# Performance work log

Measured on AMD Instinct MI355X. Metric: run time of the kernel, lower is better.

Reference implementation:

```python
import jax, jax.numpy as jnp
import numpy as np

B, S, D = 1, 2048, 3072
H, DH = 24, 128
ENC, NIP = 512, 64
COND = (512 // 8) * (512 // 8) * 16 // 64  # 1024 cond tokens per lora
RANK, ALPHA, LW, IP_SCALE = 16, 16.0, 1.0, 1.0
EPS = 1e-5


def _rms(x):
    return x * jax.lax.rsqrt(jnp.mean(x * x, axis=-1, keepdims=True) + EPS)


def _to_heads(x):
    b, s, _ = x.shape
    return x.reshape(b, s, H, DH).transpose(0, 2, 1, 3)  # [B,H,S,DH]


def _from_heads(x):
    b, h, s, d = x.shape
    return x.transpose(0, 2, 1, 3).reshape(b, s, h * d)


def _lora(x, dn, up):
    # token mask keeps only the cond block (number=0, n_loras=1 -> last COND tokens)
    y = ((x[:, -COND:, :] @ dn) @ up) * (ALPHA / RANK)
    z = jnp.zeros((x.shape[0], x.shape[1] - COND, up.shape[1]), x.dtype)
    return jnp.concatenate([z, y], axis=1)


def _sdpa(q, k, v, mask=None):
    s = jnp.einsum('bhqd,bhkd->bhqk', q, k) * (1.0 / np.sqrt(DH))
    if mask is not None:
        s = s + mask
    return jnp.einsum('bhqk,bhkd->bhqd', jax.nn.softmax(s, axis=-1), v)


def _forward(hidden_states, encoder_hidden_states, image_emb,
             Wq, bq, Wk, bk, Wv, bv, Waq, baq, Wak, bak, Wav, bav,
             Wo, bo, Wao, bao, Wkip, Wvip,
             lq_dn, lq_up, lk_dn, lk_up, lv_dn, lv_up, lp_dn, lp_up):
    hs, ehs, img = hidden_states, encoder_hidden_states, image_emb
    # context (encoder) projections + RMSNorm on q/k
    eq = _rms(_to_heads(ehs @ Waq + baq))
    ek = _rms(_to_heads(ehs @ Wak + bak))
    ev = _to_heads(ehs @ Wav + bav)
    # main-stream q/k/v with masked LoRA branches
    q = hs @ Wq + bq + LW * _lora(hs, lq_dn, lq_up)
    k = hs @ Wk + bk + LW * _lora(hs, lk_dn, lk_up)
    v = hs @ Wv + bv + LW * _lora(hs, lv_dn, lv_up)
    q = _rms(_to_heads(q))
    k = _rms(_to_heads(k))
    v = _to_heads(v)
    # IP-adapter branch: extra K/V from image_emb, norm_added_k is RMSNorm(128)
    kip = _rms(_to_heads(img @ Wkip))
    vip = _to_heads(img @ Wvip)
    ip_out = _from_heads(_sdpa(q, kip, vip))  # [B,S,D]
    # concat encoder stream ahead of main stream
    q = jnp.concatenate([eq, q], axis=2)
    k = jnp.concatenate([ek, k], axis=2)
    v = jnp.concatenate([ev, v], axis=2)
    SL = ENC + S
    SB = SL - COND  # scaled_block_size
    m = jnp.ones((SL, SL), jnp.float32)
    m = m.at[:SB, :].set(0.0)        # non-cond rows attend everywhere
    m = m.at[SB:, SB:].set(0.0)      # single cond block attends to itself (n_loras=1)
    mask = m * (-1e20)
    out = _from_heads(_sdpa(q, k, v, mask))  # [B,SL,D]
    enc_out = out[:, :ENC, :]
    main = out[:, ENC:, :] + IP_SCALE * ip_out
    main = main @ Wo + bo
    main = main + LW * _lora(main, lp_dn, lp_up)  # proj LoRA (to_out dropout=identity)
    enc_out = enc_out @ Wao + bao
    return jnp.concatenate([enc_out, main], axis=1)  # [B, ENC+S, D]


def setup_inputs():
    key = jax.random.key(0)
    ks = iter(jax.random.split(key, 40))
    w = lambda *sh: jax.random.normal(next(ks), sh, jnp.float32) * 0.02
    return dict(
        hidden_states=jax.random.normal(next(ks), (B, S, D), jnp.float32),
        encoder_hidden_states=jax.random.normal(next(ks), (B, ENC, D), jnp.float32),
        image_emb=jax.random.normal(next(ks), (B, NIP, D), jnp.float32),
        Wq=w(D, D), bq=w(D), Wk=w(D, D), bk=w(D), Wv=w(D, D), bv=w(D),
        Waq=w(D, D), baq=w(D), Wak=w(D, D), bak=w(D), Wav=w(D, D), bav=w(D),
        Wo=w(D, D), bo=w(D), Wao=w(D, D), bao=w(D),
        Wkip=w(D, D), Wvip=w(D, D),
        lq_dn=w(D, RANK), lq_up=w(RANK, D), lk_dn=w(D, RANK), lk_up=w(RANK, D),
        lv_dn=w(D, RANK), lv_up=w(RANK, D), lp_dn=w(D, RANK), lp_up=w(RANK, D),
    )


def reference(hidden_states, encoder_hidden_states, image_emb,
              Wq, bq, Wk, bk, Wv, bv, Waq, baq, Wak, bak, Wav, bav,
              Wo, bo, Wao, bao, Wkip, Wvip,
              lq_dn, lq_up, lk_dn, lk_up, lv_dn, lv_up, lp_dn, lp_up):
    return _forward(hidden_states, encoder_hidden_states, image_emb,
                    Wq, bq, Wk, bk, Wv, bv, Waq, baq, Wak, bak, Wav, bav,
                    Wo, bo, Wao, bao, Wkip, Wvip,
                    lq_dn, lq_up, lk_dn, lk_up, lv_dn, lv_up, lp_dn, lp_up)
```

## Files before the change

### kernel.cpp

```cpp
#include <hip/hip_runtime.h>

typedef unsigned short u16;
typedef short s16x8 __attribute__((ext_vector_type(8)));
typedef float f32x4 __attribute__((ext_vector_type(4)));
typedef const __attribute__((address_space(1))) unsigned int* as1_u32p;
typedef __attribute__((address_space(3))) unsigned int* as3_u32p;

static_assert(sizeof(s16x8) == 16, "");

struct alignas(8) U16x4 { u16 x, y, z, w; };

__device__ __forceinline__ u16 f2bf(float f) {
  union { float f; unsigned u; } c; c.f = f;
  return (u16)((c.u + 0x7fffu + ((c.u >> 16) & 1u)) >> 16);
}
__device__ __forceinline__ float bf2f(u16 h) {
  union { unsigned u; float f; } c; c.u = ((unsigned)h) << 16;
  return c.f;
}
__device__ __forceinline__ void async16(const void* g, void* l) {
  __builtin_amdgcn_global_load_lds((as1_u32p)g, (as3_u32p)l, 16, 0, 0);
}

__launch_bounds__(256)
__global__ void mega_prep(const float* __restrict__ Waq, const float* __restrict__ Wak,
                          const float* __restrict__ Wav, const float* __restrict__ Wq,
                          const float* __restrict__ Wk, const float* __restrict__ Wv,
                          u16* __restrict__ WTbE, u16* __restrict__ WTbM,
                          const float* __restrict__ Wo, const float* __restrict__ bo,
                          const float* __restrict__ lp_dn, float* __restrict__ Wod,
                          const float* __restrict__ d0, const float* __restrict__ d1,
                          const float* __restrict__ d2, float* __restrict__ tl,
                          const float* __restrict__ hs, u16* __restrict__ hsb,
                          const float* __restrict__ ehs, u16* __restrict__ ehsb,
                          const float* __restrict__ img, u16* __restrict__ imgb,
                          const float* __restrict__ baq, const float* __restrict__ bak,
                          const float* __restrict__ bav, const float* __restrict__ bq,
                          const float* __restrict__ bk, const float* __restrict__ bv,
                          float* __restrict__ bpk,
                          const float* __restrict__ u0, const float* __restrict__ u1,
                          const float* __restrict__ u2) {
  __shared__ char lmem[16896];
  const int b = blockIdx.x;
  const int tid = threadIdx.x;
  if (b < 13824) {
    int mat = b / 2304, tile = b % 2304;
    const float* src = (mat == 0) ? Waq : (mat == 1) ? Wak : (mat == 2) ? Wav
                       : (mat == 3) ? Wq : (mat == 4) ? Wk : Wv;
    u16* dst = (mat < 3) ? WTbE + (long)mat * 3072 * 3072
                         : WTbM + (long)(mat - 3) * 3072 * 3136;
    const int ldd = (mat < 3) ? 3072 : 3136;
    float (*tile2)[32][33] = (float(*)[32][33])lmem;
    int k0 = (tile / 96) * 128, n0 = (tile % 96) * 32;
    int r = tid >> 3, c4 = (tid & 7) * 4;
    float4 v[4];
#pragma unroll
    for (int t = 0; t < 4; ++t)
      v[t] = *(const float4*)(src + (long)(k0 + 32 * t + r) * 3072 + n0 + c4);
#pragma unroll
    for (int t = 0; t < 4; ++t) {
      tile2[t][r][c4 + 0] = v[t].x; tile2[t][r][c4 + 1] = v[t].y;
      tile2[t][r][c4 + 2] = v[t].z; tile2[t][r][c4 + 3] = v[t].w;
    }
    __syncthreads();
#pragma unroll
    for (int t = 0; t < 4; ++t) {
      U16x4 o{f2bf(tile2[t][c4 + 0][r]), f2bf(tile2[t][c4 + 1][r]),
              f2bf(tile2[t][c4 + 2][r]), f2bf(tile2[t][c4 + 3][r])};
      *(U16x4*)(dst + (long)(n0 + r) * ldd + k0 + 32 * t + c4) = o;
    }
  } else if (b < 14848) {
    const int m = b - 13824;
    float (*red)[48] = (float(*)[48])lmem;
    const float* xr = hs + (long)(1024 + m) * 3072;
    float p[48];
#pragma unroll
    for (int r = 0; r < 48; ++r) p[r] = 0.f;
    for (int k = tid; k < 3072; k += 256) {
      float a = xr[k];
      const float* e0 = d0 + (long)k * 16;
      const float* e1 = d1 + (long)k * 16;
      const float* e2 = d2 + (long)k * 16;
#pragma unroll
      for (int r = 0; r < 16; ++r) {
        p[r]      += a * e0[r];
        p[16 + r] += a * e1[r];
        p[32 + r] += a * e2[r];
      }
    }
#pragma unroll
    for (int r = 0; r < 48; ++r)
#pragma unroll
      for (int st = 1; st < 64; st <<= 1) p[r] += __shfl_xor(p[r], st, 64);
    int lane = tid & 63, w = tid >> 6;
    if (lane == 0) {
#pragma unroll
      for (int r = 0; r < 48; ++r) red[w][r] = p[r];
    }
    __syncthreads();
    if (tid < 48) {
      int r = tid;
      tl[(long)m * 48 + r] = red[0][r] + red[1][r] + red[2][r] + red[3][r];
    }
  } else if (b < 17921) {
    const int m = b - 14848;
    float (*red)[16] = (float(*)[16])lmem;
    const float* xr = (m < 3072) ? Wo + (long)m * 3072 : bo;
    float p[16];
#pragma unroll
    for (int r = 0; r < 16; ++r) p[r] = 0.f;
    for (int k = tid; k < 3072; k += 256) {
      float a = xr[k];
      const float* d = lp_dn + (long)k * 16;
#pragma unroll
      for (int r = 0; r < 16; ++r) p[r] += a * d[r];
    }
#pragma unroll
    for (int r = 0; r < 16; ++r)
#pragma unroll
      for (int st = 1; st < 64; st <<= 1) p[r] += __shfl_xor(p[r], st, 64);
    int lane = tid & 63, w = tid >> 6;
    if (lane == 0) {
#pragma unroll
      for (int r = 0; r < 16; ++r) red[w][r] = p[r];
    }
    __syncthreads();
    if (tid < 16) {
      int r = tid;
      Wod[(long)m * 16 + r] = red[0][r] + red[1][r] + red[2][r] + red[3][r];
    }
  } else {
    const int pb = b - 17921;
    if (pb < 3136) {
      long idx = (long)pb * 256 + tid;
      long m = idx / 392, c = idx % 392;
      U16x4 o0{0, 0, 0, 0}, o1{0, 0, 0, 0};
      if (c < 384) {
        const float* p = hs + m * 3072 + c * 8;
        float4 a = *(const float4*)p;
        float4 bb = *(const float4*)(p + 4);
        o0 = U16x4{f2bf(a.x), f2bf(a.y), f2bf(a.z), f2bf(a.w)};
        o1 = U16x4{f2bf(bb.x), f2bf(bb.y), f2bf(bb.z), f2bf(bb.w)};
      }
      u16* d = hsb + m * 3136 + c * 8;
      *(U16x4*)d = o0;
      *(U16x4*)(d + 4) = o1;
    } else if (pb < 3904) {
      long i = ((long)(pb - 3136) * 256 + tid) * 8;
      float4 a = *(const float4*)(ehs + i);
      float4 bb = *(const float4*)(ehs + i + 4);
      *(U16x4*)(ehsb + i) = U16x4{f2bf(a.x), f2bf(a.y), f2bf(a.z), f2bf(a.w)};
      *(U16x4*)(ehsb + i + 4) = U16x4{f2bf(bb.x), f2bf(bb.y), f2bf(bb.z), f2bf(bb.w)};
    } else if (pb < 4000) {
      long i = ((long)(pb - 3904) * 256 + tid) * 8;
      float4 a = *(const float4*)(img + i);
      float4 bb = *(const float4*)(img + i + 4);
      *(U16x4*)(imgb + i) = U16x4{f2bf(a.x), f2bf(a.y), f2bf(a.z), f2bf(a.w)};
      *(U16x4*)(imgb + i + 4) = U16x4{f2bf(bb.x), f2bf(bb.y), f2bf(bb.z), f2bf(bb.w)};
    } else if (pb < 4072) {
      int i = (pb - 4000) * 256 + tid;
      if (i < 9216)
        bpk[i] = (i < 3072) ? baq[i] : (i < 6144) ? bak[i - 3072] : bav[i - 6144];
      else {
        int j = i - 9216;
        bpk[i] = (j < 3072) ? bq[j] : (j < 6144) ? bk[j - 3072] : bv[j - 6144];
      }
    } else {
      int idx = (pb - 4072) * 256 + tid;
      int n = idx >> 6, i = idx & 63;
      int seg = n / 3072;
      const float* up = (seg == 0) ? u0 : (seg == 1) ? u1 : u2;
      int r = i - seg * 16;
      float v = (r >= 0 && r < 16) ? up[(long)r * 3072 + (n - seg * 3072)] : 0.f;
      WTbM[(long)n * 3136 + 3072 + i] = f2bf(v);
    }
  }
}

__launch_bounds__(256)
__global__ void t_hs(const float* __restrict__ tl, u16* __restrict__ hsb) {
  int idx = blockIdx.x * 256 + threadIdx.x;
  int m = idx / 48, r = idx % 48;
  hsb[(long)(1024 + m) * 3136 + 3072 + r] = f2bf(tl[m * 48 + r]);
}

__launch_bounds__(256)
__global__ void transpose_kv(const float* __restrict__ Wkip, const float* __restrict__ Wvip,
                             u16* __restrict__ E1) {
  __shared__ float tile2[4][32][33];
  const int b = blockIdx.x;
  int mat = b / 2304, tile = b % 2304;
  const float* src = mat ? Wvip : Wkip;
  u16* dst = E1 + (long)mat * 3072 * 3072;
  const int tid = threadIdx.x;
  int k0 = (tile / 96) * 128, n0 = (tile % 96) * 32;
  int r = tid >> 3, c4 = (tid & 7) * 4;
  float4 v[4];
#pragma unroll
  for (int t = 0; t < 4; ++t)
    v[t] = *(const float4*)(src + (long)(k0 + 32 * t + r) * 3072 + n0 + c4);
#pragma unroll
  for (int t = 0; t < 4; ++t) {
    tile2[t][r][c4 + 0] = v[t].x; tile2[t][r][c4 + 1] = v[t].y;
    tile2[t][r][c4 + 2] = v[t].z; tile2[t][r][c4 + 3] = v[t].w;
  }
  __syncthreads();
#pragma unroll
  for (int t = 0; t < 4; ++t) {
    U16x4 o{f2bf(tile2[t][c4 + 0][r]), f2bf(tile2[t][c4 + 1][r]),
            f2bf(tile2[t][c4 + 2][r]), f2bf(tile2[t][c4 + 3][r])};
    *(U16x4*)(dst + (long)(n0 + r) * 3072 + k0 + 32 * t + c4) = o;
  }
}

template <int BM, int MI, int NI>
__launch_bounds__(256)
__global__ void gemm_f32(const u16* __restrict__ A, int lda,
                         const u16* __restrict__ B, int ldb,
                         float* __restrict__ C, int ldc,
                         const float* __restrict__ bias, int KC, long cstride) {
  constexpr int WCOLS = 128 / (NI * 16);
  constexpr int ABYTES = BM * 128;
  __shared__ char smem[ABYTES + 128 * 128];
  char* As = smem;
  char* Bs = smem + ABYTES;
  const int tid = threadIdx.x;
  const int w = tid >> 6, lane = tid & 63;
  const int lr = lane & 15, lg = lane >> 4;
  const int wr = w / WCOLS, wc = w % WCOLS;
  const int nbx = gridDim.x;
  const int nwg = nbx * gridDim.y;
  const int flat = blockIdx.y * nbx + blockIdx.x;
  const int swz = (flat & 7) * (nwg >> 3) + (flat >> 3);
  const long m0 = (long)(swz % nbx) * BM;
  const long n0 = (long)(swz / nbx) * 128;
  const int k0 = blockIdx.z * KC;
  C += blockIdx.z * cstride;
  f32x4 acc[MI][NI] = {};
  constexpr int ACH = BM / 32;
  for (int kb = k0; kb < k0 + KC; kb += 64) {
    __syncthreads();
#pragma unroll
    for (int i = 0; i < ACH; ++i) {
      int x = (tid + 256 * i) * 16;
      int row = x >> 7;
      int sx = x ^ ((row & 7) << 4);
      async16((const char*)(A + (m0 + row) * lda + kb) + (sx & 127),
              As + ((w << 10) + (i << 12)));
    }
#pragma unroll
    for (int i = 0; i < 4; ++i) {
      int x = (tid + 256 * i) * 16;
      int row = x >> 7;
      int sx = x ^ ((row & 7) << 4);
      async16((const char*)(B + (n0 + row) * ldb + kb) + (sx & 127),
              Bs + ((w << 10) + (i << 12)));
    }
    __syncthreads();
#pragma unroll
    for (int kc = 0; kc < 2; ++kc) {
      s16x8 af[MI], bfr[NI];
#pragma unroll
      for (int mi = 0; mi < MI; ++mi) {
        int row = wr * (MI * 16) + mi * 16 + lr;
        int b = ((row << 7) + kc * 64 + lg * 16) ^ ((row & 7) << 4);
        af[mi] = *(const s16x8*)(As + b);
      }
#pragma unroll
      for (int ni = 0; ni < NI; ++ni) {
        int row = wc * (NI * 16) + ni * 16 + lr;
        int b = ((row << 7) + kc * 64 + lg * 16) ^ ((row & 7) << 4);
        bfr[ni] = *(const s16x8*)(Bs + b);
      }
#pragma unroll
      for (int mi = 0; mi < MI; ++mi)
#pragma unroll
        for (int ni = 0; ni < NI; ++ni)
          acc[mi][ni] = __builtin_amdgcn_mfma_f32_16x16x32_bf16(af[mi], bfr[ni], acc[mi][ni], 0, 0, 0);
    }
  }
#pragma unroll
  for (int mi = 0; mi < MI; ++mi) {
#pragma unroll
    for (int ni = 0; ni < NI; ++ni) {
      long col = n0 + wc * (NI * 16) + ni * 16 + lr;
      float bv = bias ? bias[col] : 0.f;
#pragma unroll
      for (int j = 0; j < 4; ++j) {
        long row = m0 + wr * (MI * 16) + mi * 16 + lg * 4 + j;
        C[row * ldc + col] = acc[mi][ni][j] + bv;
      }
    }
  }
}

__launch_bounds__(256)
__global__ void rms_ip(const float* __restrict__ in, u16* __restrict__ Ko,
                       u16* __restrict__ VipT) {
  const int t = blockIdx.x & 63;
  const int vhalf = blockIdx.x >> 6;
  const int col0 = vhalf ? 3072 : 0;
  const int w = threadIdx.x >> 6, lane = threadIdx.x & 63;
  const long ps = 64LL * 6144;
#pragma unroll
  for (int hh = 0; hh < 6; ++hh) {
    int h = w * 6 + hh;
    const float* x = in + (long)t * 6144 + col0 + h * 128 + lane * 2;
    float a = x[0] + x[ps] + x[2 * ps] + x[3 * ps];
    float b = x[1] + x[1 + ps] + x[1 + 2 * ps] + x[1 + 3 * ps];
    if (!vhalf) {
      float ss = a * a + b * b;
#pragma unroll
      for (int st = 1; st < 64; st <<= 1) ss += __shfl_xor(ss, st, 64);
      float scale = rsqrtf(ss * (1.f / 128.f) + 1e-5f);
      unsigned pa = f2bf(a * scale), pb = f2bf(b * scale);
      *(unsigned*)(Ko + ((long)h * 64 + t) * 128 + lane * 2) = pa | (pb << 16);
    } else {
      VipT[((long)h * 128 + lane * 2) * 64 + t] = f2bf(a);
      VipT[((long)h * 128 + lane * 2 + 1) * 64 + t] = f2bf(b);
    }
  }
}

__launch_bounds__(256, 3)
__global__ void gemm_qkv(const u16* __restrict__ Aenc, const u16* __restrict__ Amain,
                         const u16* __restrict__ Benc, const u16* __restrict__ Bmain,
                         u16* __restrict__ Qo, u16* __restrict__ Ko, u16* __restrict__ VTo,
                         const float* __restrict__ bpk) {
  __shared__ char smem[32768];
  char* As = smem;
  char* Bs = smem + 16384;
  const int tid = threadIdx.x;
  const int w = tid >> 6, lane = tid & 63;
  const int lr = lane & 15, lg = lane >> 4;
  const int wr = w >> 1, wc = w & 1;
  const int flat = blockIdx.y * 20 + blockIdx.x;
  const int swz = (flat & 7) * 180 + (flat >> 3);
  const int mx = swz % 20;
  const long n0 = (long)(swz / 20) * 128;
  const u16* A;
  const u16* B;
  const float* bias;
  int lda, ldb, K, t0;
  long m0;
  if (mx < 4) {
    A = Aenc; lda = 3072; B = Benc; ldb = 3072; K = 3072; t0 = 0;
    m0 = (long)mx * 128; bias = bpk;
  } else {
    A = Amain; lda = 3136; B = Bmain; ldb = 3136; K = 3136; t0 = 512;
    m0 = (long)(mx - 4) * 128; bias = bpk + 9216;
  }
  f32x4 acc[4][4] = {};
  for (int kb = 0; kb < K; kb += 64) {
    __syncthreads();
#pragma unroll
    for (int i = 0; i < 4; ++i) {
      int x = (tid + 256 * i) * 16;
      int row = x >> 7;
      int sx = (x & 127) ^ ((row & 7) << 4);
      async16((const char*)(A + (m0 + row) * lda + kb) + sx, As + x);
    }
#pragma unroll
    for (int i = 0; i < 4; ++i) {
      int x = (tid + 256 * i) * 16;
      int row = x >> 7;
      int sx = (x & 127) ^ ((row & 7) << 4);
      async16((const char*)(B + (n0 + row) * ldb + kb) + sx, Bs + x);
    }
    __syncthreads();
#pragma unroll
    for (int kc = 0; kc < 2; ++kc) {
      s16x8 af[4], bfr[4];
#pragma unroll
      for (int mi = 0; mi < 4; ++mi) {
        int row = wr * 64 + mi * 16 + lr;
        af[mi] = *(const s16x8*)(As + (row << 7) + ((kc * 64 + lg * 16) ^ ((row & 7) << 4)));
      }
#pragma unroll
      for (int ni = 0; ni < 4; ++ni) {
        int row = wc * 64 + ni * 16 + lr;
        bfr[ni] = *(const s16x8*)(Bs + (row << 7) + ((kc * 64 + lg * 16) ^ ((row & 7) << 4)));
      }
#pragma unroll
      for (int mi = 0; mi < 4; ++mi)
#pragma unroll
        for (int ni = 0; ni < 4; ++ni)
          acc[mi][ni] = __builtin_amdgcn_mfma_f32_16x16x32_bf16(af[mi], bfr[ni], acc[mi][ni], 0, 0, 0);
    }
  }
  const int seg = (int)(n0 / 3072);
  const int head = (int)((n0 % 3072) >> 7);
#pragma unroll
  for (int ni = 0; ni < 4; ++ni) {
    float bv = bias[n0 + wc * 64 + ni * 16 + lr];
#pragma unroll
    for (int mi = 0; mi < 4; ++mi)
#pragma unroll
      for (int j = 0; j < 4; ++j) acc[mi][ni][j] += bv;
  }
  __syncthreads();
  float scl[4][4];
  if (seg < 2) {
    float* red = (float*)smem;
#pragma unroll
    for (int mi = 0; mi < 4; ++mi)
#pragma unroll
      for (int j = 0; j < 4; ++j) {
        float s = 0.f;
#pragma unroll
        for (int ni = 0; ni < 4; ++ni) s += acc[mi][ni][j] * acc[mi][ni][j];
#pragma unroll
        for (int st = 1; st < 16; st <<= 1) s += __shfl_xor(s, st, 16);
        if (lr == 0) red[(wr * 64 + mi * 16 + lg * 4 + j) * 2 + wc] = s;
        scl[mi][j] = s;
      }
    __syncthreads();
#pragma unroll
    for (int mi = 0; mi < 4; ++mi)
#pragma unroll
      for (int j = 0; j < 4; ++j) {
        int row = wr * 64 + mi * 16 + lg * 4 + j;
        float t = red[row * 2] + red[row * 2 + 1];
        scl[mi][j] = rsqrtf(t * (1.f / 128.f) + 1e-5f);
      }
    __syncthreads();
  }
  if (seg < 2) {
#pragma unroll
    for (int mi = 0; mi < 4; ++mi)
#pragma unroll
      for (int ni = 0; ni < 4; ++ni) {
        int d2 = (wc * 64 + ni * 16 + lr) * 2;
#pragma unroll
        for (int j = 0; j < 4; ++j) {
          int tok = wr * 64 + mi * 16 + lg * 4 + j;
          *(u16*)(smem + tok * 256 + (d2 ^ ((tok & 7) << 4))) =
              f2bf(acc[mi][ni][j] * scl[mi][j]);
        }
      }
  } else {
#pragma unroll
    for (int mi = 0; mi < 4; ++mi)
#pragma unroll
      for (int ni = 0; ni < 4; ++ni) {
        int d = wc * 64 + ni * 16 + lr;
        int tok0b = (wr * 64 + mi * 16 + lg * 4) * 2;
        U16x4 o{f2bf(acc[mi][ni][0]), f2bf(acc[mi][ni][1]),
                f2bf(acc[mi][ni][2]), f2bf(acc[mi][ni][3])};
        *(U16x4*)(smem + d * 256 + (tok0b ^ ((d & 7) << 4))) = o;
      }
  }
  __syncthreads();
#pragma unroll
  for (int i = 0; i < 8; ++i) {
    int x = (tid + 256 * i) * 16;
    int row = x >> 8, col = x & 255;
    s16x8 vdat = *(const s16x8*)(smem + row * 256 + (col ^ ((row & 7) << 4)));
    if (seg < 2) {
      u16* g = (seg == 0 ? Qo : Ko) + ((long)head * 2560 + t0 + m0 + row) * 128;
      *(s16x8*)((char*)g + col) = vdat;
    } else {
      u16* g = VTo + ((long)head * 128 + row) * 2560 + t0 + m0;
      *(s16x8*)((char*)g + col) = vdat;
    }
  }
}

__launch_bounds__(512, 2)
__global__ void attn_mega(const u16* __restrict__ QB, const u16* __restrict__ KB,
                          const u16* __restrict__ VT, const u16* __restrict__ KipB,
                          const u16* __restrict__ VipT, u16* __restrict__ OutTok,
                          const float* __restrict__ Wao, const float* __restrict__ Wo,
                          u16* __restrict__ WTbE, u16* __restrict__ WTbM,
                          const float* __restrict__ lp_up) {
  __shared__ char smem[81920];
  const int bf = blockIdx.x;
  const int tid = threadIdx.x;
  if (bf >= 480) {
    if (bf < 2784) {
      int t2 = (bf - 480) * 2 + (tid >> 8);
      int mat = t2 / 2304, tile = t2 % 2304;
      const float* src = mat ? Wo : Wao;
      u16* dst = mat ? WTbM : WTbE;
      const int ldd = mat ? 3136 : 3072;
      float (*tl4)[4][32][33] = (float(*)[4][32][33])smem;
      int half = tid >> 8, lt = tid & 255;
      int k0 = (tile / 96) * 128, n0t = (tile % 96) * 32;
      int r = lt >> 3, c4 = (lt & 7) * 4;
      float4 v[4];
#pragma unroll
      for (int t = 0; t < 4; ++t)
        v[t] = *(const float4*)(src + (long)(k0 + 32 * t + r) * 3072 + n0t + c4);
#pragma unroll
      for (int t = 0; t < 4; ++t) {
        tl4[half][t][r][c4 + 0] = v[t].x; tl4[half][t][r][c4 + 1] = v[t].y;
        tl4[half][t][r][c4 + 2] = v[t].z; tl4[half][t][r][c4 + 3] = v[t].w;
      }
      __syncthreads();
#pragma unroll
      for (int t = 0; t < 4; ++t) {
        U16x4 o{f2bf(tl4[half][t][c4 + 0][r]), f2bf(tl4[half][t][c4 + 1][r]),
                f2bf(tl4[half][t][c4 + 2][r]), f2bf(tl4[half][t][c4 + 3][r])};
        *(U16x4*)(dst + (long)(n0t + r) * ldd + k0 + 32 * t + c4) = o;
      }
    } else {
      int idx = (bf - 2784) * 512 + tid;
      int n = idx >> 6, i = idx & 63;
      float v = (i < 16) ? lp_up[(long)i * 3072 + n] : 0.f;
      WTbM[(long)n * 3136 + 3072 + i] = f2bf(v);
    }
    return;
  }
  const int w = tid >> 6, lane = tid & 63;
  const int lr = lane & 15, lg = lane >> 4;
  int h, qb;
  if (bf < 288) { h = bf / 12; qb = bf % 12; }
  else { int s = bf - 288; h = s / 8; qb = 12 + s % 8; }
  const int q0 = qb * 128;
  const bool ip = (q0 >= 512);
  const u16* Qrow = QB + (long)(h * 2560 + q0 + w * 16 + lr) * 128;
  s16x8 qf[4];
#pragma unroll
  for (int dc = 0; dc < 4; ++dc) qf[dc] = *(const s16x8*)(Qrow + dc * 32 + lg * 8);
  f32x4 accO[8] = {};
  float l_r[4] = {0.f, 0.f, 0.f, 0.f};
  const int kv0 = (q0 >= 1536) ? 1536 : 0;
  const float sc = 0.08838834764831845f;

  auto stage_main = [&](int kv, int buf) {
#pragma unroll
    for (int i = 0; i < 2; ++i) {
      int x = (tid + 512 * i) * 16;
      int row = x >> 8;
      int sx = x ^ ((row & 7) << 4);
      async16((const char*)(KB + (long)(h * 2560 + kv + row) * 128) + (sx & 255),
              smem + buf * 16384 + ((i << 13) + (w << 10)));
    }
#pragma unroll
    for (int i = 0; i < 2; ++i) {
      int x = (tid + 512 * i) * 16;
      int row = x >> 7;
      int sx = x ^ ((row & 7) << 4);
      async16((const char*)(VT + (long)(h * 128 + row) * 2560 + kv) + (sx & 127),
              smem + 32768 + buf * 16384 + ((i << 13) + (w << 10)));
    }
  };
  auto stage_ip = [&](int buf) {
#pragma unroll
    for (int i = 0; i < 2; ++i) {
      int x = (tid + 512 * i) * 16;
      int row = x >> 8;
      int sx = x ^ ((row & 7) << 4);
      async16((const char*)(KipB + (long)(h * 64 + row) * 128) + (sx & 255),
              smem + buf * 16384 + ((i << 13) + (w << 10)));
    }
#pragma unroll
    for (int i = 0; i < 2; ++i) {
      int x = (tid + 512 * i) * 16;
      int row = x >> 7;
      int sx = x ^ ((row & 7) << 4);
      async16((const char*)(VipT + (long)(h * 128 + row) * 64) + (sx & 127),
              smem + 32768 + buf * 16384 + ((i << 13) + (w << 10)));
    }
  };

  stage_main(kv0, 0);
  __syncthreads();
  int cur = 0;
  for (int kv = kv0; kv < 2560; kv += 64) {
    if (kv + 64 < 2560) stage_main(kv + 64, cur ^ 1);
    else if (ip) stage_ip(cur ^ 1);
    const char* Ks = smem + cur * 16384;
    const char* Vs = smem + 32768 + cur * 16384;
    char* Pw = smem + 65536 + w * 2048;
    f32x4 s[4] = {};
    __builtin_amdgcn_s_setprio(1);
#pragma unroll
    for (int kt = 0; kt < 4; ++kt)
#pragma unroll
      for (int dc = 0; dc < 4; ++dc) {
        int row = kt * 16 + lr;
        int b = ((row << 8) + dc * 64 + lg * 16) ^ ((row & 7) << 4);
        s16x8 kf = *(const s16x8*)(Ks + b);
        s[kt] = __builtin_amdgcn_mfma_f32_16x16x32_bf16(qf[dc], kf, s[kt], 0, 0, 0);
      }
    __builtin_amdgcn_s_setprio(0);
#pragma unroll
    for (int kt = 0; kt < 4; ++kt)
#pragma unroll
      for (int j = 0; j < 4; ++j) {
        float pv = __expf(fmaf(s[kt][j], sc, -12.0f));
        l_r[j] += pv;
        int prow = lg * 4 + j;
        int b = ((prow << 7) + (kt * 16 + lr) * 2) ^ ((prow & 7) << 4);
        *(u16*)(Pw + b) = f2bf(pv);
      }
    asm volatile("s_waitcnt lgkmcnt(0)" ::: "memory");
    __builtin_amdgcn_s_setprio(1);
#pragma unroll
    for (int kc = 0; kc < 2; ++kc) {
      int pb = ((lr << 7) + kc * 64 + lg * 16) ^ ((lr & 7) << 4);
      s16x8 pf = *(const s16x8*)(Pw + pb);
#pragma unroll
      for (int dt = 0; dt < 8; ++dt) {
        int row = dt * 16 + lr;
        int b = ((row << 7) + kc * 64 + lg * 16) ^ ((row & 7) << 4);
        s16x8 vf = *(const s16x8*)(Vs + b);
        accO[dt] = __builtin_amdgcn_mfma_f32_16x16x32_bf16(pf, vf, accO[dt], 0, 0, 0);
      }
    }
    __builtin_amdgcn_s_setprio(0);
    __syncthreads();
    cur ^= 1;
  }
#pragma unroll
  for (int j = 0; j < 4; ++j) {
#pragma unroll
    for (int st = 1; st < 16; st <<= 1) l_r[j] += __shfl_xor(l_r[j], st, 16);
    l_r[j] = 1.f / l_r[j];
  }
#pragma unroll
  for (int dt = 0; dt < 8; ++dt)
#pragma unroll
    for (int j = 0; j < 4; ++j) accO[dt][j] *= l_r[j];
  if (ip) {
    const char* Ks = smem + cur * 16384;
    const char* Vs = smem + 32768 + cur * 16384;
    char* Pw = smem + 65536 + w * 2048;
    f32x4 s2[4] = {};
#pragma unroll
    for (int kt = 0; kt < 4; ++kt)
#pragma unroll
      for (int dc = 0; dc < 4; ++dc) {
        int row = kt * 16 + lr;
        int b = ((row << 8) + dc * 64 + lg * 16) ^ ((row & 7) << 4);
        s16x8 kf = *(const s16x8*)(Ks + b);
        s2[kt] = __builtin_amdgcn_mfma_f32_16x16x32_bf16(qf[dc], kf, s2[kt], 0, 0, 0);
      }
    float p2[4][4];
    float l2[4] = {0.f, 0.f, 0.f, 0.f};
#pragma unroll
    for (int kt = 0; kt < 4; ++kt)
#pragma unroll
      for (int j = 0; j < 4; ++j) {
        float pv = __expf(fmaf(s2[kt][j], sc, -12.0f));
        p2[kt][j] = pv;
        l2[j] += pv;
      }
#pragma unroll
    for (int j = 0; j < 4; ++j) {
#pragma unroll
      for (int st = 1; st < 16; st <<= 1) l2[j] += __shfl_xor(l2[j], st, 16);
      l2[j] = 1.f / l2[j];
    }
#pragma unroll
    for (int kt = 0; kt < 4; ++kt)
#pragma unroll
      for (int j = 0; j < 4; ++j) {
        int prow = lg * 4 + j;
        int b = ((prow << 7) + (kt * 16 + lr) * 2) ^ ((prow & 7) << 4);
        *(u16*)(Pw + b) = f2bf(p2[kt][j] * l2[j]);
      }
    asm volatile("s_waitcnt lgkmcnt(0)" ::: "memory");
#pragma unroll
    for (int kc = 0; kc < 2; ++kc) {
      int pb = ((lr << 7) + kc * 64 + lg * 16) ^ ((lr & 7) << 4);
      s16x8 pf = *(const s16x8*)(Pw + pb);
#pragma unroll
      for (int dt = 0; dt < 8; ++dt) {
        int row = dt * 16 + lr;
        int b = ((row << 7) + kc * 64 + lg * 16) ^ ((row & 7) << 4);
        s16x8 vf = *(const s16x8*)(Vs + b);
        accO[dt] = __builtin_amdgcn_mfma_f32_16x16x32_bf16(pf, vf, accO[dt], 0, 0, 0);
      }
    }
  }
#pragma unroll
  for (int j = 0; j < 4; ++j) {
    long tok = q0 + w * 16 + lg * 4 + j;
#pragma unroll
    for (int dt = 0; dt < 8; ++dt) {
      long col = h * 128 + dt * 16 + lr;
      OutTok[tok * 3136 + col] = f2bf(accO[dt][j]);
    }
  }
}

__launch_bounds__(256)
__global__ void t_tail(u16* __restrict__ At, const float* __restrict__ Wod) {
  __shared__ float red[4][16];
  const int tok = blockIdx.x;
  u16* tail = At + (long)(512 + tok) * 3136 + 3072;
  if (tok < 1024) {
    if (threadIdx.x < 64) tail[threadIdx.x] = 0;
    return;
  }
  const u16* xr = At + (long)(512 + tok) * 3136;
  float p[16];
#pragma unroll
  for (int r = 0; r < 16; ++r) p[r] = 0.f;
  for (int n = threadIdx.x; n < 3072; n += 256) {
    float a = bf2f(xr[n]);
    const float* wd = Wod + (long)n * 16;
#pragma unroll
    for (int r = 0; r < 16; ++r) p[r] += a * wd[r];
  }
#pragma unroll
  for (int r = 0; r < 16; ++r)
#pragma unroll
    for (int st = 1; st < 64; st <<= 1) p[r] += __shfl_xor(p[r], st, 64);
  int lane = threadIdx.x & 63, w = threadIdx.x >> 6;
  if (lane == 0) {
#pragma unroll
    for (int r = 0; r < 16; ++r) red[w][r] = p[r];
  }
  __syncthreads();
  if (threadIdx.x < 64) {
    if (threadIdx.x < 16) {
      int r = threadIdx.x;
      float t = red[0][r] + red[1][r] + red[2][r] + red[3][r] + Wod[3072L * 16 + r];
      tail[r] = f2bf(t);
    } else {
      tail[threadIdx.x] = 0;
    }
  }
}

__launch_bounds__(256)
__global__ void gemm_out(const u16* __restrict__ Atok, const u16* __restrict__ Benc,
                         const u16* __restrict__ Bmain, float* __restrict__ outp,
                         const float* __restrict__ bao, const float* __restrict__ bo) {
  __shared__ char smem[128 * 128 + 128 * 128];
  char* As = smem;
  char* Bs = smem + 128 * 128;
  const int tid = threadIdx.x;
  const int w = tid >> 6, lane = tid & 63;
  const int lr = lane & 15, lg = lane >> 4;
  const int wr = w >> 1, wc = w & 1;
  const int flat = blockIdx.y * 20 + blockIdx.x;
  const int swz = (flat & 7) * 60 + (flat >> 3);
  const int mx = swz % 20;
  const long n0 = (long)(swz / 20) * 128;
  const u16* A;
  const u16* B;
  const float* bias;
  float* C;
  int ldb, K;
  long m0;
  if (mx < 4) {
    A = Atok; B = Benc; ldb = 3072; K = 3072; bias = bao; C = outp;
    m0 = (long)mx * 128;
  } else {
    A = Atok + 512L * 3136; B = Bmain; ldb = 3136; K = 3136; bias = bo;
    C = outp + 512L * 3072; m0 = (long)(mx - 4) * 128;
  }
  f32x4 acc[4][4] = {};
  for (int kb = 0; kb < K; kb += 64) {
    __syncthreads();
#pragma unroll
    for (int i = 0; i < 4; ++i) {
      int x = (tid + 256 * i) * 16;
      int row = x >> 7;
      int sx = x ^ ((row & 7) << 4);
      async16((const char*)(A + (m0 + row) * 3136 + kb) + (sx & 127),
              As + ((w << 10) + (i << 12)));
    }
#pragma unroll
    for (int i = 0; i < 4; ++i) {
      int x = (tid + 256 * i) * 16;
      int row = x >> 7;
      int sx = x ^ ((row & 7) << 4);
      async16((const char*)(B + (n0 + row) * ldb + kb) + (sx & 127),
              Bs + ((w << 10) + (i << 12)));
    }
    __syncthreads();
#pragma unroll
    for (int kc = 0; kc < 2; ++kc) {
      s16x8 af[4], bfr[4];
#pragma unroll
      for (int mi = 0; mi < 4; ++mi) {
        int row = wr * 64 + mi * 16 + lr;
        int b = ((row << 7) + kc * 64 + lg * 16) ^ ((row & 7) << 4);
        af[mi] = *(const s16x8*)(As + b);
      }
#pragma unroll
      for (int ni = 0; ni < 4; ++ni) {
        int row = wc * 64 + ni * 16 + lr;
        int b = ((row << 7) + kc * 64 + lg * 16) ^ ((row & 7) << 4);
        bfr[ni] = *(const s16x8*)(Bs + b);
      }
#pragma unroll
      for (int mi = 0; mi < 4; ++mi)
#pragma unroll
        for (int ni = 0; ni < 4; ++ni)
          acc[mi][ni] = __builtin_amdgcn_mfma_f32_16x16x32_bf16(af[mi], bfr[ni], acc[mi][ni], 0, 0, 0);
    }
  }
#pragma unroll
  for (int mi = 0; mi < 4; ++mi) {
#pragma unroll
    for (int ni = 0; ni < 4; ++ni) {
      long col = n0 + wc * 64 + ni * 16 + lr;
      float bv = bias[col];
#pragma unroll
      for (int j = 0; j < 4; ++j) {
        long row = m0 + wr * 64 + mi * 16 + lg * 4 + j;
        C[row * 3072 + col] = acc[mi][ni][j] + bv;
      }
    }
  }
}


extern "C" void kernel_launch(void* const* d_in, const int* in_sizes, int n_in,
                              void* d_out, int out_size, void* d_ws, size_t ws_size,
                              hipStream_t stream) {
  const float* hs    = (const float*)d_in[0];
  const float* ehs   = (const float*)d_in[1];
  const float* img   = (const float*)d_in[2];
  const float* Wq    = (const float*)d_in[3];
  const float* bq    = (const float*)d_in[4];
  const float* Wk    = (const float*)d_in[5];
  const float* bk    = (const float*)d_in[6];
  const float* Wv    = (const float*)d_in[7];
  const float* bv    = (const float*)d_in[8];
  const float* Waq   = (const float*)d_in[9];
  const float* baq   = (const float*)d_in[10];
  const float* Wak   = (const float*)d_in[11];
  const float* bak   = (const float*)d_in[12];
  const float* Wav   = (const float*)d_in[13];
  const float* bav   = (const float*)d_in[14];
  const float* Wo    = (const float*)d_in[15];
  const float* bo    = (const float*)d_in[16];
  const float* Wao   = (const float*)d_in[17];
  const float* bao   = (const float*)d_in[18];
  const float* Wkip  = (const float*)d_in[19];
  const float* Wvip  = (const float*)d_in[20];
  const float* lq_dn = (const float*)d_in[21];
  const float* lq_up = (const float*)d_in[22];
  const float* lk_dn = (const float*)d_in[23];
  const float* lk_up = (const float*)d_in[24];
  const float* lv_dn = (const float*)d_in[25];
  const float* lv_up = (const float*)d_in[26];
  const float* lp_dn = (const float*)d_in[27];
  const float* lp_up = (const float*)d_in[28];
  float* outp = (float*)d_out;

  char* ws = (char*)d_ws;
  size_t off = 0;
  auto take = [&](size_t b) { char* p = ws + off; off += (b + 255) & ~(size_t)255; return p; };
  u16*   WTbE = (u16*)take(3LL * 3072 * 3072 * 2);
  u16*   WTbM = (u16*)take(3LL * 3072 * 3136 * 2);
  u16*   hsb  = (u16*)take(2048LL * 3136 * 2);
  u16*   ehsb = (u16*)take(512LL * 3072 * 2);
  u16*   imgb = (u16*)take(64LL * 3072 * 2);
  u16*   VTf  = (u16*)take(24LL * 128 * 2560 * 2);
  float* IP0  = (float*)take(4LL * 64 * 6144 * 4);
  u16*   KipB = (u16*)take(24LL * 64 * 128 * 2);
  u16*   VipT = (u16*)take(24LL * 128 * 64 * 2);
  float* bpk  = (float*)take(2 * 9216 * 4);
  float* tl   = (float*)take(1024LL * 48 * 4);
  float* Wod  = (float*)take(3073LL * 16 * 4);
  u16* QBf = (u16*)d_out;
  u16* KBf = (u16*)d_out + 24LL * 2560 * 128;
  u16* AttnTok = hsb;
  u16* E1 = WTbE + 3072LL * 3072;

  mega_prep<<<24297, 256, 0, stream>>>(Waq, Wak, Wav, Wq, Wk, Wv, WTbE, WTbM,
                                       Wo, bo, lp_dn, Wod,
                                       lq_dn, lk_dn, lv_dn, tl,
                                       hs, hsb, ehs, ehsb, img, imgb,
                                       baq, bak, bav, bq, bk, bv, bpk,
                                       lq_up, lk_up, lv_up);
  t_hs<<<192, 256, 0, stream>>>(tl, hsb);

  gemm_qkv<<<dim3(20, 72), 256, 0, stream>>>(ehsb, hsb, WTbE, WTbM, QBf, KBf, VTf, bpk);

  transpose_kv<<<4608, 256, 0, stream>>>(Wkip, Wvip, E1);

  gemm_f32<64, 4, 2><<<dim3(1, 48, 4), 256, 0, stream>>>(imgb, 3072, E1, 3072, IP0, 6144,
                                                          nullptr, 768, 64LL * 6144);
  rms_ip<<<128, 256, 0, stream>>>(IP0, KipB, VipT);

  attn_mega<<<3168, 512, 0, stream>>>(QBf, KBf, VTf, KipB, VipT, AttnTok,
                                      Wao, Wo, WTbE, WTbM, lp_up);

  t_tail<<<2048, 256, 0, stream>>>(AttnTok, Wod);

  gemm_out<<<dim3(20, 24), 256, 0, stream>>>(AttnTok, WTbE, WTbM, outp, bao, bo);
}
```

Baseline: 565.8 us.

## Enlarge weight-transpose tiles to 128x128 and double IP GEMM split-K

The fp32-to-bf16 weight transposes in mega_prep, transpose_kv and the attn_mega tail now process 128x128 tiles per block instead of 128x32, using a larger shared-memory buffer. This cuts block counts roughly fourfold, lowering per-block launch and scheduling overhead, and gives each thread more loads in flight. Separately, the IP K/V GEMM's split-K factor goes from 4 to 8, with rms_ip summing eight partials. The larger shared allocation (about 66 KB) may reduce occupancy and slow the other branches of mega_prep that share that declaration.

```diff
diff --git a/kernel.cpp b/kernel.cpp
--- a/kernel.cpp
+++ b/kernel.cpp
@@ -40,37 +40,43 @@
                           float* __restrict__ bpk,
                           const float* __restrict__ u0, const float* __restrict__ u1,
                           const float* __restrict__ u2) {
-  __shared__ char lmem[16896];
+  __shared__ char lmem[67584];
   const int b = blockIdx.x;
   const int tid = threadIdx.x;
-  if (b < 13824) {
-    int mat = b / 2304, tile = b % 2304;
+  if (b < 3456) {
+    int mat = b / 576, tile = b % 576;
     const float* src = (mat == 0) ? Waq : (mat == 1) ? Wak : (mat == 2) ? Wav
                        : (mat == 3) ? Wq : (mat == 4) ? Wk : Wv;
     u16* dst = (mat < 3) ? WTbE + (long)mat * 3072 * 3072
                          : WTbM + (long)(mat - 3) * 3072 * 3136;
     const int ldd = (mat < 3) ? 3072 : 3136;
-    float (*tile2)[32][33] = (float(*)[32][33])lmem;
-    int k0 = (tile / 96) * 128, n0 = (tile % 96) * 32;
+    float (*t2)[4][32][33] = (float(*)[4][32][33])lmem;
+    int k0 = (tile / 24) * 128, n0 = (tile % 24) * 128;
     int r = tid >> 3, c4 = (tid & 7) * 4;
-    float4 v[4];
-#pragma unroll
-    for (int t = 0; t < 4; ++t)
-      v[t] = *(const float4*)(src + (long)(k0 + 32 * t + r) * 3072 + n0 + c4);
-#pragma unroll
-    for (int t = 0; t < 4; ++t) {
-      tile2[t][r][c4 + 0] = v[t].x; tile2[t][r][c4 + 1] = v[t].y;
-      tile2[t][r][c4 + 2] = v[t].z; tile2[t][r][c4 + 3] = v[t].w;
-    }
-    __syncthreads();
-#pragma unroll
-    for (int t = 0; t < 4; ++t) {
-      U16x4 o{f2bf(tile2[t][c4 + 0][r]), f2bf(tile2[t][c4 + 1][r]),
-              f2bf(tile2[t][c4 + 2][r]), f2bf(tile2[t][c4 + 3][r])};
-      *(U16x4*)(dst + (long)(n0 + r) * ldd + k0 + 32 * t + c4) = o;
-    }
-  } else if (b < 14848) {
-    const int m = b - 13824;
+    float4 v[4][4];
+#pragma unroll
+    for (int i = 0; i < 4; ++i)
+#pragma unroll
+      for (int j = 0; j < 4; ++j)
+        v[i][j] = *(const float4*)(src + (long)(k0 + i * 32 + r) * 3072 + n0 + j * 32 + c4);
+#pragma unroll
+    for (int i = 0; i < 4; ++i)
+#pragma unroll
+      for (int j = 0; j < 4; ++j) {
+        t2[i][j][r][c4 + 0] = v[i][j].x; t2[i][j][r][c4 + 1] = v[i][j].y;
+        t2[i][j][r][c4 + 2] = v[i][j].z; t2[i][j][r][c4 + 3] = v[i][j].w;
+      }
+    __syncthreads();
+#pragma unroll
+    for (int j = 0; j < 4; ++j)
+#pragma unroll
+      for (int i = 0; i < 4; ++i) {
+        U16x4 o{f2bf(t2[i][j][c4 + 0][r]), f2bf(t2[i][j][c4 + 1][r]),
+                f2bf(t2[i][j][c4 + 2][r]), f2bf(t2[i][j][c4 + 3][r])};
+        *(U16x4*)(dst + (long)(n0 + j * 32 + r) * ldd + k0 + i * 32 + c4) = o;
+      }
+  } else if (b < 4480) {
+    const int m = b - 3456;
     float (*red)[48] = (float(*)[48])lmem;
     const float* xr = hs + (long)(1024 + m) * 3072;
     float p[48];
@@ -102,8 +108,8 @@
       int r = tid;
       tl[(long)m * 48 + r] = red[0][r] + red[1][r] + red[2][r] + red[3][r];
     }
-  } else if (b < 17921) {
-    const int m = b - 14848;
+  } else if (b < 7553) {
+    const int m = b - 4480;
     float (*red)[16] = (float(*)[16])lmem;
     const float* xr = (m < 3072) ? Wo + (long)m * 3072 : bo;
     float p[16];
@@ -130,7 +136,7 @@
       Wod[(long)m * 16 + r] = red[0][r] + red[1][r] + red[2][r] + red[3][r];
     }
   } else {
-    const int pb = b - 17921;
+    const int pb = b - 7553;
     if (pb < 3136) {
       long idx = (long)pb * 256 + tid;
       long m = idx / 392, c = idx % 392;
@@ -187,30 +193,36 @@
 __launch_bounds__(256)
 __global__ void transpose_kv(const float* __restrict__ Wkip, const float* __restrict__ Wvip,
                              u16* __restrict__ E1) {
-  __shared__ float tile2[4][32][33];
+  __shared__ float t2[4][4][32][33];
   const int b = blockIdx.x;
-  int mat = b / 2304, tile = b % 2304;
+  int mat = b / 576, tile = b % 576;
   const float* src = mat ? Wvip : Wkip;
   u16* dst = E1 + (long)mat * 3072 * 3072;
   const int tid = threadIdx.x;
-  int k0 = (tile / 96) * 128, n0 = (tile % 96) * 32;
+  int k0 = (tile / 24) * 128, n0 = (tile % 24) * 128;
   int r = tid >> 3, c4 = (tid & 7) * 4;
-  float4 v[4];
-#pragma unroll
-  for (int t = 0; t < 4; ++t)
-    v[t] = *(const float4*)(src + (long)(k0 + 32 * t + r) * 3072 + n0 + c4);
-#pragma unroll
-  for (int t = 0; t < 4; ++t) {
-    tile2[t][r][c4 + 0] = v[t].x; tile2[t][r][c4 + 1] = v[t].y;
-    tile2[t][r][c4 + 2] = v[t].z; tile2[t][r][c4 + 3] = v[t].w;
-  }
+  float4 v[4][4];
+#pragma unroll
+  for (int i = 0; i < 4; ++i)
+#pragma unroll
+    for (int j = 0; j < 4; ++j)
+      v[i][j] = *(const float4*)(src + (long)(k0 + i * 32 + r) * 3072 + n0 + j * 32 + c4);
+#pragma unroll
+  for (int i = 0; i < 4; ++i)
+#pragma unroll
+    for (int j = 0; j < 4; ++j) {
+      t2[i][j][r][c4 + 0] = v[i][j].x; t2[i][j][r][c4 + 1] = v[i][j].y;
+      t2[i][j][r][c4 + 2] = v[i][j].z; t2[i][j][r][c4 + 3] = v[i][j].w;
+    }
   __syncthreads();
 #pragma unroll
-  for (int t = 0; t < 4; ++t) {
-    U16x4 o{f2bf(tile2[t][c4 + 0][r]), f2bf(tile2[t][c4 + 1][r]),
-            f2bf(tile2[t][c4 + 2][r]), f2bf(tile2[t][c4 + 3][r])};
-    *(U16x4*)(dst + (long)(n0 + r) * 3072 + k0 + 32 * t + c4) = o;
-  }
+  for (int j = 0; j < 4; ++j)
+#pragma unroll
+    for (int i = 0; i < 4; ++i) {
+      U16x4 o{f2bf(t2[i][j][c4 + 0][r]), f2bf(t2[i][j][c4 + 1][r]),
+              f2bf(t2[i][j][c4 + 2][r]), f2bf(t2[i][j][c4 + 3][r])};
+      *(U16x4*)(dst + (long)(n0 + j * 32 + r) * 3072 + k0 + i * 32 + c4) = o;
+    }
 }
 
 template <int BM, int MI, int NI>
@@ -306,8 +318,12 @@
   for (int hh = 0; hh < 6; ++hh) {
     int h = w * 6 + hh;
     const float* x = in + (long)t * 6144 + col0 + h * 128 + lane * 2;
-    float a = x[0] + x[ps] + x[2 * ps] + x[3 * ps];
-    float b = x[1] + x[1 + ps] + x[1 + 2 * ps] + x[1 + 3 * ps];
+    float a = 0.f, b = 0.f;
+#pragma unroll
+    for (int z = 0; z < 8; ++z) {
+      a += x[z * ps];
+      b += x[1 + z * ps];
+    }
     if (!vhalf) {
       float ss = a * a + b * b;
 #pragma unroll
@@ -477,34 +493,43 @@
   const int bf = blockIdx.x;
   const int tid = threadIdx.x;
   if (bf >= 480) {
-    if (bf < 2784) {
-      int t2 = (bf - 480) * 2 + (tid >> 8);
-      int mat = t2 / 2304, tile = t2 % 2304;
+    if (bf < 1632) {
+      int t2i = bf - 480;
+      int mat = t2i / 576, tile = t2i % 576;
       const float* src = mat ? Wo : Wao;
       u16* dst = mat ? WTbM : WTbE;
       const int ldd = mat ? 3136 : 3072;
-      float (*tl4)[4][32][33] = (float(*)[4][32][33])smem;
+      float (*t2)[4][32][33] = (float(*)[4][32][33])smem;
+      int k0 = (tile / 24) * 128, n0t = (tile % 24) * 128;
       int half = tid >> 8, lt = tid & 255;
-      int k0 = (tile / 96) * 128, n0t = (tile % 96) * 32;
       int r = lt >> 3, c4 = (lt & 7) * 4;
-      float4 v[4];
-#pragma unroll
-      for (int t = 0; t < 4; ++t)
-        v[t] = *(const float4*)(src + (long)(k0 + 32 * t + r) * 3072 + n0t + c4);
-#pragma unroll
-      for (int t = 0; t < 4; ++t) {
-        tl4[half][t][r][c4 + 0] = v[t].x; tl4[half][t][r][c4 + 1] = v[t].y;
-        tl4[half][t][r][c4 + 2] = v[t].z; tl4[half][t][r][c4 + 3] = v[t].w;
-      }
+      float4 v[2][4];
+#pragma unroll
+      for (int ii = 0; ii < 2; ++ii)
+#pragma unroll
+        for (int j = 0; j < 4; ++j)
+          v[ii][j] = *(const float4*)(src + (long)(k0 + (half * 2 + ii) * 32 + r) * 3072 +
+                                      n0t + j * 32 + c4);
+#pragma unroll
+      for (int ii = 0; ii < 2; ++ii)
+#pragma unroll
+        for (int j = 0; j < 4; ++j) {
+          int i = half * 2 + ii;
+          t2[i][j][r][c4 + 0] = v[ii][j].x; t2[i][j][r][c4 + 1] = v[ii][j].y;
+          t2[i][j][r][c4 + 2] = v[ii][j].z; t2[i][j][r][c4 + 3] = v[ii][j].w;
+        }
       __syncthreads();
 #pragma unroll
-      for (int t = 0; t < 4; ++t) {
-        U16x4 o{f2bf(tl4[half][t][c4 + 0][r]), f2bf(tl4[half][t][c4 + 1][r]),
-                f2bf(tl4[half][t][c4 + 2][r]), f2bf(tl4[half][t][c4 + 3][r])};
-        *(U16x4*)(dst + (long)(n0t + r) * ldd + k0 + 32 * t + c4) = o;
-      }
+      for (int jj = 0; jj < 2; ++jj)
+#pragma unroll
+        for (int i = 0; i < 4; ++i) {
+          int j = half * 2 + jj;
+          U16x4 o{f2bf(t2[i][j][c4 + 0][r]), f2bf(t2[i][j][c4 + 1][r]),
+                  f2bf(t2[i][j][c4 + 2][r]), f2bf(t2[i][j][c4 + 3][r])};
+          *(U16x4*)(dst + (long)(n0t + j * 32 + r) * ldd + k0 + i * 32 + c4) = o;
+        }
     } else {
-      int idx = (bf - 2784) * 512 + tid;
+      int idx = (bf - 1632) * 512 + tid;
       int n = idx >> 6, i = idx & 63;
       float v = (i < 16) ? lp_up[(long)i * 3072 + n] : 0.f;
       WTbM[(long)n * 3136 + 3072 + i] = f2bf(v);
@@ -855,7 +880,7 @@
   u16*   ehsb = (u16*)take(512LL * 3072 * 2);
   u16*   imgb = (u16*)take(64LL * 3072 * 2);
   u16*   VTf  = (u16*)take(24LL * 128 * 2560 * 2);
-  float* IP0  = (float*)take(4LL * 64 * 6144 * 4);
+  float* IP0  = (float*)take(8LL * 64 * 6144 * 4);
   u16*   KipB = (u16*)take(24LL * 64 * 128 * 2);
   u16*   VipT = (u16*)take(24LL * 128 * 64 * 2);
   float* bpk  = (float*)take(2 * 9216 * 4);
@@ -866,7 +891,7 @@
   u16* AttnTok = hsb;
   u16* E1 = WTbE + 3072LL * 3072;
 
-  mega_prep<<<24297, 256, 0, stream>>>(Waq, Wak, Wav, Wq, Wk, Wv, WTbE, WTbM,
+  mega_prep<<<13929, 256, 0, stream>>>(Waq, Wak, Wav, Wq, Wk, Wv, WTbE, WTbM,
                                        Wo, bo, lp_dn, Wod,
                                        lq_dn, lk_dn, lv_dn, tl,
                                        hs, hsb, ehs, ehsb, img, imgb,
@@ -876,13 +901,13 @@
 
   gemm_qkv<<<dim3(20, 72), 256, 0, stream>>>(ehsb, hsb, WTbE, WTbM, QBf, KBf, VTf, bpk);
 
-  transpose_kv<<<4608, 256, 0, stream>>>(Wkip, Wvip, E1);
-
-  gemm_f32<64, 4, 2><<<dim3(1, 48, 4), 256, 0, stream>>>(imgb, 3072, E1, 3072, IP0, 6144,
-                                                          nullptr, 768, 64LL * 6144);
+  transpose_kv<<<1152, 256, 0, stream>>>(Wkip, Wvip, E1);
+
+  gemm_f32<64, 4, 2><<<dim3(1, 48, 8), 256, 0, stream>>>(imgb, 3072, E1, 3072, IP0, 6144,
+                                                          nullptr, 384, 64LL * 6144);
   rms_ip<<<128, 256, 0, stream>>>(IP0, KipB, VipT);
 
-  attn_mega<<<3168, 512, 0, stream>>>(QBf, KBf, VTf, KipB, VipT, AttnTok,
+  attn_mega<<<2016, 512, 0, stream>>>(QBf, KBf, VTf, KipB, VipT, AttnTok,
                                       Wao, Wo, WTbE, WTbM, lp_up);
 
   t_tail<<<2048, 256, 0, stream>>>(AttnTok, Wod);
```

New measurement: 570.2 us (median of 3 runs). Within noise of the previous version (+0.8%).
